# Optimization experiments

Measured on AMD Instinct MI355X. Metric: run time of the kernel, lower is better.

The kernel has to match this reference:

```python
import jax, jax.numpy as jnp
import numpy as np

H, W, C_IN, C_ADD = 721, 1440, 78, 8
N_NODES, K = 5882, 128
DAY_OF_YEAR = 182.5  # module default time_of_year
LN_EPS = 1e-5        # haiku LayerNorm default
NORM_EPS = 1e-7


def setup_inputs() -> dict:
    key = jax.random.key(0)
    ks = jax.random.split(key, 4)
    return {
        "var_grid": jax.random.normal(ks[0], (H, W, C_IN), dtype=jnp.float32),
        "nearby_idx": jax.random.randint(ks[1], (N_NODES, K), 0, H * W),
        "input_means": jnp.zeros((C_IN + C_ADD,), jnp.float32),
        "input_stds": jnp.ones((C_IN + C_ADD,), jnp.float32),
        "W1": jax.random.normal(ks[2], (C_IN + C_ADD, 256), dtype=jnp.float32) * 0.1,
        "b1": jnp.zeros((256,), jnp.float32),
        "ln_scale": jnp.ones((256,), jnp.float32),
        "ln_offset": jnp.zeros((256,), jnp.float32),
        "W2": jax.random.normal(ks[3], (256, 256), dtype=jnp.float32) * 0.1,
        "b2": jnp.zeros((256,), jnp.float32),
    }


def _additional_features(h, w):
    # 8 extra channels: sin/cos of lat/lon, normalized day-of-year, 3 zero pads
    lat = jnp.linspace(-90.0, 90.0, h)
    lon = jnp.linspace(0.0, 360.0, w)
    lat2d = jnp.broadcast_to(lat[:, None], (h, w))
    lon2d = jnp.broadcast_to(lon[None, :], (h, w))
    lat_r, lon_r = jnp.radians(lat2d), jnp.radians(lon2d)
    day = jnp.float32(DAY_OF_YEAR / 365.0)
    z = jnp.zeros((h, w), jnp.float32)
    return jnp.stack([
        jnp.sin(lat_r), jnp.cos(lat_r), jnp.sin(lon_r), jnp.cos(lon_r),
        jnp.full((h, w), day, jnp.float32), z, z, z,
    ], axis=-1)  # [H, W, 8]


def reference(var_grid, nearby_idx, input_means, input_stds,
              W1, b1, ln_scale, ln_offset, W2, b2):
    h, w, c = var_grid.shape
    add = _additional_features(h, w)                       # [H, W, 8]
    flat = jnp.concatenate([var_grid, add], -1).reshape(h * w, c + C_ADD)
    gathered = flat[nearby_idx]                            # [N, K, 86] irregular gather
    x = (gathered - input_means) / (input_stds + NORM_EPS)
    hidden = jax.nn.relu(jnp.einsum('nkc,cd->nkd', x, W1) + b1)
    mu = hidden.mean(-1, keepdims=True)
    var = hidden.var(-1, keepdims=True)
    hidden = (hidden - mu) * jax.lax.rsqrt(var + LN_EPS) * ln_scale + ln_offset
    nodes = jnp.einsum('nkd,de->nke', hidden, W2) + b2     # [N, K, 256]
    return nodes
```

## Files before the change

kernel.cpp:

```cpp
#include <hip/hip_runtime.h>
#include <hip/hip_bf16.h>
#include <math.h>

#define GH 721
#define GW 1440
#define C_IN 78
#define NNODES 5882
#define KNEIGH 128
#define M_TOTAL (NNODES * KNEIGH)
#define TM 64
#define NBLOCKS (M_TOTAL / TM)

typedef __attribute__((ext_vector_type(8))) short bf16x8;
typedef __attribute__((ext_vector_type(4))) float f32x4;

__device__ __forceinline__ unsigned short f2bf(float x) {
    __hip_bfloat16 b = __float2bfloat16(x);
    union { __hip_bfloat16 h; unsigned short u; } cv; cv.h = b; return cv.u;
}

__global__ void prep_kernel(const float* __restrict__ W1, const float* __restrict__ W2,
                            const float* __restrict__ means, const float* __restrict__ stds,
                            const float* __restrict__ b1,
                            unsigned short* __restrict__ bp1, unsigned short* __restrict__ bp2,
                            float* __restrict__ latT, float* __restrict__ lonT,
                            float* __restrict__ b1p)
{
    const int NB1 = 3 * 4 * 256 * 8;
    const int NB2 = 8 * 4 * 256 * 8;
    const int NTOT = NB1 + NB2 + GH + GW + 256;
    for (int e = blockIdx.x * blockDim.x + threadIdx.x; e < NTOT;
         e += gridDim.x * blockDim.x) {
        if (e < NB1) {
            int j = e & 7, c = (e >> 3) & 255, o = (e >> 11) & 3, s = e >> 13;
            int k = s * 32 + o * 8 + j;
            float v = 0.f;
            if (k < 82) v = W1[k * 256 + c] / (stds[k] + 1e-7f);
            bp1[e] = f2bf(v);
        } else if (e < NB1 + NB2) {
            int t = e - NB1;
            int j = t & 7, c = (t >> 3) & 255, o = (t >> 11) & 3, s = t >> 13;
            int k = s * 32 + o * 8 + j;
            bp2[t] = f2bf(W2[k * 256 + c]);
        } else if (e < NB1 + NB2 + GH) {
            int h = e - NB1 - NB2;
            float r = (-90.f + 0.25f * (float)h) * 0.017453292519943295f;
            latT[2 * h]     = sinf(r);
            latT[2 * h + 1] = cosf(r);
        } else if (e < NB1 + NB2 + GH + GW) {
            int w = e - NB1 - NB2 - GH;
            float r = ((float)w * (360.f / 1439.f)) * 0.017453292519943295f;
            lonT[2 * w]     = sinf(r);
            lonT[2 * w + 1] = cosf(r);
        } else {
            int c = e - NB1 - NB2 - GH - GW;
            float acc = b1[c];
            #pragma unroll 1
            for (int k = 0; k < 86; ++k) {
                float inv = 1.f / (stds[k] + 1e-7f);
                float w = W1[k * 256 + c] * inv;
                acc -= means[k] * w;
                if (k == 82) acc += 0.5f * w;
            }
            b1p[c] = acc;
        }
    }
}

__global__ __launch_bounds__(256, 4)
void fused_kernel(const float* __restrict__ var_grid, const int* __restrict__ idxs,
                  const unsigned short* __restrict__ bp1, const unsigned short* __restrict__ bp2,
                  const float* __restrict__ latT, const float* __restrict__ lonT,
                  const float* __restrict__ b1p, const float* __restrict__ lnS,
                  const float* __restrict__ lnO, const float* __restrict__ b2,
                  float* __restrict__ out)
{
    __shared__ __align__(16) char smem[TM * 256 * 2];
    __shared__ float red[2][4][TM];
    unsigned short* h_lds = (unsigned short*)smem;
    unsigned short (*x_lds)[104] = (unsigned short (*)[104])smem;
    float* otile = (float*)smem;

    const int tid  = threadIdx.x;
    const int lane = tid & 63;
    const int wave = tid >> 6;
    const int l15  = lane & 15;
    const int lg   = lane >> 4;
    const int wbase = wave * 64;
    const long block0 = (long)blockIdx.x * TM;

    {
        const int row = tid >> 2, p = tid & 3;
        const int idx = idxs[block0 + row];
        const int hh = idx / GW;
        const int ww = idx - hh * GW;
        const float* src = var_grid + (long)idx * C_IN;
        unsigned int* xrow = (unsigned int*)&x_lds[row][0];
        #pragma unroll
        for (int t = 0; t < 12; ++t) {
            const int q = p + 4 * t;
            float v0, v1;
            if (q < 39) {
                float2 t2 = *(const float2*)(src + 2 * q);
                v0 = t2.x; v1 = t2.y;
            } else if (q == 39) { v0 = latT[2 * hh]; v1 = latT[2 * hh + 1]; }
            else if (q == 40)   { v0 = lonT[2 * ww]; v1 = lonT[2 * ww + 1]; }
            else                { v0 = 0.f; v1 = 0.f; }
            xrow[q] = ((unsigned int)f2bf(v1) << 16) | (unsigned int)f2bf(v0);
        }
    }

    float b1v[4], lsv[4], lov[4], b2v[4];
    #pragma unroll
    for (int nf = 0; nf < 4; ++nf) {
        int col = wbase + nf * 16 + l15;
        b1v[nf] = b1p[col]; lsv[nf] = lnS[col]; lov[nf] = lnO[col]; b2v[nf] = b2[col];
    }
    __syncthreads();

    f32x4 acc[4][4];
    #pragma unroll
    for (int mf = 0; mf < 4; ++mf)
        #pragma unroll
        for (int nf = 0; nf < 4; ++nf) acc[mf][nf] = (f32x4){0.f, 0.f, 0.f, 0.f};

    #pragma unroll
    for (int s = 0; s < 3; ++s) {
        bf16x8 af[4], bw[4];
        #pragma unroll
        for (int mf = 0; mf < 4; ++mf)
            af[mf] = *(const bf16x8*)&x_lds[mf * 16 + l15][s * 32 + lg * 8];
        #pragma unroll
        for (int nf = 0; nf < 4; ++nf)
            bw[nf] = *(const bf16x8*)(bp1 + ((size_t)((s * 4 + lg) * 256) + wbase + nf * 16 + l15) * 8);
        #pragma unroll
        for (int mf = 0; mf < 4; ++mf)
            #pragma unroll
            for (int nf = 0; nf < 4; ++nf)
                acc[mf][nf] = __builtin_amdgcn_mfma_f32_16x16x32_bf16(af[mf], bw[nf], acc[mf][nf], 0, 0, 0);
    }

    float sm[4][4], sq[4][4];
    #pragma unroll
    for (int mf = 0; mf < 4; ++mf)
        #pragma unroll
        for (int i = 0; i < 4; ++i) { sm[mf][i] = 0.f; sq[mf][i] = 0.f; }

    #pragma unroll
    for (int mf = 0; mf < 4; ++mf)
        #pragma unroll
        for (int nf = 0; nf < 4; ++nf)
            #pragma unroll
            for (int i = 0; i < 4; ++i) {
                float v = fmaxf(acc[mf][nf][i] + b1v[nf], 0.f);
                acc[mf][nf][i] = v;
                sm[mf][i] += v;
                sq[mf][i] += v * v;
            }

    #pragma unroll
    for (int m = 1; m < 16; m <<= 1)
        #pragma unroll
        for (int mf = 0; mf < 4; ++mf)
            #pragma unroll
            for (int i = 0; i < 4; ++i) {
                sm[mf][i] += __shfl_xor(sm[mf][i], m, 64);
                sq[mf][i] += __shfl_xor(sq[mf][i], m, 64);
            }

    if (l15 == 0) {
        #pragma unroll
        for (int mf = 0; mf < 4; ++mf)
            #pragma unroll
            for (int i = 0; i < 4; ++i) {
                int row = mf * 16 + lg * 4 + i;
                red[0][wave][row] = sm[mf][i];
                red[1][wave][row] = sq[mf][i];
            }
    }
    __syncthreads();

    #pragma unroll
    for (int mf = 0; mf < 4; ++mf)
        #pragma unroll
        for (int i = 0; i < 4; ++i) {
            int row = mf * 16 + lg * 4 + i;
            float tot = red[0][0][row] + red[0][1][row] + red[0][2][row] + red[0][3][row];
            float tq  = red[1][0][row] + red[1][1][row] + red[1][2][row] + red[1][3][row];
            float mean = tot * (1.f / 256.f);
            float var  = tq * (1.f / 256.f) - mean * mean;
            float rs = rsqrtf(var + 1e-5f);
            #pragma unroll
            for (int nf = 0; nf < 4; ++nf) {
                float v = (acc[mf][nf][i] - mean) * rs * lsv[nf] + lov[nf];
                int col = wbase + nf * 16 + l15;
                unsigned off = (unsigned)(row * 512 + col * 2);
                off ^= (unsigned)((row & 7) << 4);
                *(unsigned short*)((char*)h_lds + off) = f2bf(v);
            }
        }
    __syncthreads();

    #pragma unroll
    for (int mf = 0; mf < 4; ++mf)
        #pragma unroll
        for (int nf = 0; nf < 4; ++nf) acc[mf][nf] = (f32x4){0.f, 0.f, 0.f, 0.f};

    #pragma unroll
    for (int s = 0; s < 8; ++s) {
        bf16x8 af[4], bw[4];
        #pragma unroll
        for (int mf = 0; mf < 4; ++mf) {
            int row = mf * 16 + l15;
            unsigned off = (unsigned)(row * 512 + (s * 32 + lg * 8) * 2);
            off ^= (unsigned)((row & 7) << 4);
            af[mf] = *(const bf16x8*)((char*)h_lds + off);
        }
        #pragma unroll
        for (int nf = 0; nf < 4; ++nf)
            bw[nf] = *(const bf16x8*)(bp2 + ((size_t)((s * 4 + lg) * 256) + wbase + nf * 16 + l15) * 8);
        #pragma unroll
        for (int mf = 0; mf < 4; ++mf)
            #pragma unroll
            for (int nf = 0; nf < 4; ++nf)
                acc[mf][nf] = __builtin_amdgcn_mfma_f32_16x16x32_bf16(af[mf], bw[nf], acc[mf][nf], 0, 0, 0);
    }

    #pragma unroll
    for (int p = 0; p < 2; ++p) {
        __syncthreads();
        #pragma unroll
        for (int mfl = 0; mfl < 2; ++mfl) {
            const int mf = p * 2 + mfl;
            #pragma unroll
            for (int i = 0; i < 4; ++i) {
                int rl = mfl * 16 + lg * 4 + i;
                #pragma unroll
                for (int nf = 0; nf < 4; ++nf)
                    otile[rl * 256 + wbase + nf * 16 + l15] = acc[mf][nf][i] + b2v[nf];
            }
        }
        __syncthreads();
        #pragma unroll
        for (int r8 = 0; r8 < 8; ++r8) {
            const int rl = wave * 8 + r8;
            const long row_g = block0 + p * 32 + rl;
            f32x4 v = *(const f32x4*)&otile[rl * 256 + lane * 4];
            __builtin_nontemporal_store(v, (f32x4*)(out + row_g * 256 + lane * 4));
        }
    }
}

extern "C" void kernel_launch(void* const* d_in, const int* in_sizes, int n_in,
                              void* d_out, int out_size, void* d_ws, size_t ws_size,
                              hipStream_t stream) {
    const float* var_grid = (const float*)d_in[0];
    const int*   idxs     = (const int*)d_in[1];
    const float* means    = (const float*)d_in[2];
    const float* stds     = (const float*)d_in[3];
    const float* W1       = (const float*)d_in[4];
    const float* b1       = (const float*)d_in[5];
    const float* lnS      = (const float*)d_in[6];
    const float* lnO      = (const float*)d_in[7];
    const float* W2       = (const float*)d_in[8];
    const float* b2       = (const float*)d_in[9];
    float* out = (float*)d_out;

    char* ws = (char*)d_ws;
    unsigned short* bp1 = (unsigned short*)ws;
    unsigned short* bp2 = (unsigned short*)(ws + 49152);
    float* latT = (float*)(ws + 180224);
    float* lonT = (float*)(ws + 186000);
    float* b1p  = (float*)(ws + 197520);

    prep_kernel<<<362, 256, 0, stream>>>(W1, W2, means, stds, b1, bp1, bp2, latT, lonT, b1p);
    fused_kernel<<<NBLOCKS, 256, 0, stream>>>(var_grid, idxs, bp1, bp2, latT, lonT,
                                              b1p, lnS, lnO, b2, out);
}
```

Measured before the change: 484.9 us.

## Double row tile to 128 with 8-wave 2x4 grid and prefetch weight fragments

Each block now handles 128 gathered rows with 512 threads arranged as a 2x4 wave grid, so weight fragments are reused across more rows per block. Gather loads are issued into registers before the bf16 packing, and weight fragments are register double-buffered across the k-steps of both GEMMs. The output staging tile gets a rotation swizzle to reduce LDS bank conflicts. The launch bound of (512,4) asks for 8 waves per SIMD, which tightens the per-thread register budget while each thread still holds a 64-float accumulator plus prefetch buffers, so spills are a risk.

```diff
diff --git a/kernel.cpp b/kernel.cpp
--- a/kernel.cpp
+++ b/kernel.cpp
@@ -8,7 +8,7 @@
 #define NNODES 5882
 #define KNEIGH 128
 #define M_TOTAL (NNODES * KNEIGH)
-#define TM 64
+#define TM 128
 #define NBLOCKS (M_TOTAL / TM)
 
 typedef __attribute__((ext_vector_type(8))) short bf16x8;
@@ -67,7 +67,7 @@
     }
 }
 
-__global__ __launch_bounds__(256, 4)
+__global__ __launch_bounds__(512, 4)
 void fused_kernel(const float* __restrict__ var_grid, const int* __restrict__ idxs,
                   const unsigned short* __restrict__ bp1, const unsigned short* __restrict__ bp2,
                   const float* __restrict__ latT, const float* __restrict__ lonT,
@@ -84,9 +84,12 @@
     const int tid  = threadIdx.x;
     const int lane = tid & 63;
     const int wave = tid >> 6;
+    const int wr   = wave >> 2;
+    const int wc   = wave & 3;
     const int l15  = lane & 15;
     const int lg   = lane >> 4;
-    const int wbase = wave * 64;
+    const int wbase = wc * 64;
+    const int rbase = wr * 64;
     const long block0 = (long)blockIdx.x * TM;
 
     {
@@ -95,17 +98,24 @@
         const int hh = idx / GW;
         const int ww = idx - hh * GW;
         const float* src = var_grid + (long)idx * C_IN;
+        float2 g[10];
+        #pragma unroll
+        for (int t = 0; t < 10; ++t) {
+            const int q = p + 4 * t;
+            if (q < 39) g[t] = *(const float2*)(src + 2 * q);
+        }
+        float2 tail;
+        tail.x = latT[2 * hh]; tail.y = latT[2 * hh + 1];
+        float2 tail2; tail2.x = lonT[2 * ww]; tail2.y = lonT[2 * ww + 1];
         unsigned int* xrow = (unsigned int*)&x_lds[row][0];
         #pragma unroll
         for (int t = 0; t < 12; ++t) {
             const int q = p + 4 * t;
             float v0, v1;
-            if (q < 39) {
-                float2 t2 = *(const float2*)(src + 2 * q);
-                v0 = t2.x; v1 = t2.y;
-            } else if (q == 39) { v0 = latT[2 * hh]; v1 = latT[2 * hh + 1]; }
-            else if (q == 40)   { v0 = lonT[2 * ww]; v1 = lonT[2 * ww + 1]; }
-            else                { v0 = 0.f; v1 = 0.f; }
+            if (q < 39)      { v0 = g[t].x; v1 = g[t].y; }
+            else if (q == 39){ v0 = tail.x;  v1 = tail.y; }
+            else if (q == 40){ v0 = tail2.x; v1 = tail2.y; }
+            else             { v0 = 0.f; v1 = 0.f; }
             xrow[q] = ((unsigned int)f2bf(v1) << 16) | (unsigned int)f2bf(v0);
         }
     }
@@ -124,20 +134,28 @@
         #pragma unroll
         for (int nf = 0; nf < 4; ++nf) acc[mf][nf] = (f32x4){0.f, 0.f, 0.f, 0.f};
 
+    bf16x8 bw[4], bwn[4];
+    #pragma unroll
+    for (int nf = 0; nf < 4; ++nf)
+        bw[nf] = *(const bf16x8*)(bp1 + ((size_t)(lg * 256) + wbase + nf * 16 + l15) * 8);
+
     #pragma unroll
     for (int s = 0; s < 3; ++s) {
-        bf16x8 af[4], bw[4];
-        #pragma unroll
-        for (int mf = 0; mf < 4; ++mf)
-            af[mf] = *(const bf16x8*)&x_lds[mf * 16 + l15][s * 32 + lg * 8];
-        #pragma unroll
-        for (int nf = 0; nf < 4; ++nf)
-            bw[nf] = *(const bf16x8*)(bp1 + ((size_t)((s * 4 + lg) * 256) + wbase + nf * 16 + l15) * 8);
+        if (s < 2)
+            #pragma unroll
+            for (int nf = 0; nf < 4; ++nf)
+                bwn[nf] = *(const bf16x8*)(bp1 + ((size_t)(((s + 1) * 4 + lg) * 256) + wbase + nf * 16 + l15) * 8);
+        bf16x8 af[4];
+        #pragma unroll
+        for (int mf = 0; mf < 4; ++mf)
+            af[mf] = *(const bf16x8*)&x_lds[rbase + mf * 16 + l15][s * 32 + lg * 8];
         #pragma unroll
         for (int mf = 0; mf < 4; ++mf)
             #pragma unroll
             for (int nf = 0; nf < 4; ++nf)
                 acc[mf][nf] = __builtin_amdgcn_mfma_f32_16x16x32_bf16(af[mf], bw[nf], acc[mf][nf], 0, 0, 0);
+        #pragma unroll
+        for (int nf = 0; nf < 4; ++nf) bw[nf] = bwn[nf];
     }
 
     float sm[4][4], sq[4][4];
@@ -173,9 +191,9 @@
         for (int mf = 0; mf < 4; ++mf)
             #pragma unroll
             for (int i = 0; i < 4; ++i) {
-                int row = mf * 16 + lg * 4 + i;
-                red[0][wave][row] = sm[mf][i];
-                red[1][wave][row] = sq[mf][i];
+                int row = rbase + mf * 16 + lg * 4 + i;
+                red[0][wc][row] = sm[mf][i];
+                red[1][wc][row] = sq[mf][i];
             }
     }
     __syncthreads();
@@ -184,7 +202,7 @@
     for (int mf = 0; mf < 4; ++mf)
         #pragma unroll
         for (int i = 0; i < 4; ++i) {
-            int row = mf * 16 + lg * 4 + i;
+            int row = rbase + mf * 16 + lg * 4 + i;
             float tot = red[0][0][row] + red[0][1][row] + red[0][2][row] + red[0][3][row];
             float tq  = red[1][0][row] + red[1][1][row] + red[1][2][row] + red[1][3][row];
             float mean = tot * (1.f / 256.f);
@@ -207,45 +225,56 @@
         for (int nf = 0; nf < 4; ++nf) acc[mf][nf] = (f32x4){0.f, 0.f, 0.f, 0.f};
 
     #pragma unroll
+    for (int nf = 0; nf < 4; ++nf)
+        bw[nf] = *(const bf16x8*)(bp2 + ((size_t)(lg * 256) + wbase + nf * 16 + l15) * 8);
+
+    #pragma unroll
     for (int s = 0; s < 8; ++s) {
-        bf16x8 af[4], bw[4];
+        if (s < 7)
+            #pragma unroll
+            for (int nf = 0; nf < 4; ++nf)
+                bwn[nf] = *(const bf16x8*)(bp2 + ((size_t)(((s + 1) * 4 + lg) * 256) + wbase + nf * 16 + l15) * 8);
+        bf16x8 af[4];
         #pragma unroll
         for (int mf = 0; mf < 4; ++mf) {
-            int row = mf * 16 + l15;
+            int row = rbase + mf * 16 + l15;
             unsigned off = (unsigned)(row * 512 + (s * 32 + lg * 8) * 2);
             off ^= (unsigned)((row & 7) << 4);
             af[mf] = *(const bf16x8*)((char*)h_lds + off);
         }
         #pragma unroll
-        for (int nf = 0; nf < 4; ++nf)
-            bw[nf] = *(const bf16x8*)(bp2 + ((size_t)((s * 4 + lg) * 256) + wbase + nf * 16 + l15) * 8);
-        #pragma unroll
         for (int mf = 0; mf < 4; ++mf)
             #pragma unroll
             for (int nf = 0; nf < 4; ++nf)
                 acc[mf][nf] = __builtin_amdgcn_mfma_f32_16x16x32_bf16(af[mf], bw[nf], acc[mf][nf], 0, 0, 0);
-    }
-
-    #pragma unroll
-    for (int p = 0; p < 2; ++p) {
+        #pragma unroll
+        for (int nf = 0; nf < 4; ++nf) bw[nf] = bwn[nf];
+    }
+
+    #pragma unroll
+    for (int p = 0; p < 4; ++p) {
         __syncthreads();
-        #pragma unroll
-        for (int mfl = 0; mfl < 2; ++mfl) {
-            const int mf = p * 2 + mfl;
-            #pragma unroll
-            for (int i = 0; i < 4; ++i) {
-                int rl = mfl * 16 + lg * 4 + i;
+        if (wr == (p >> 1)) {
+            #pragma unroll
+            for (int mfl = 0; mfl < 2; ++mfl) {
+                const int mf = (p & 1) * 2 + mfl;
                 #pragma unroll
-                for (int nf = 0; nf < 4; ++nf)
-                    otile[rl * 256 + wbase + nf * 16 + l15] = acc[mf][nf][i] + b2v[nf];
+                for (int i = 0; i < 4; ++i) {
+                    int rl = mfl * 16 + lg * 4 + i;
+                    #pragma unroll
+                    for (int nf = 0; nf < 4; ++nf) {
+                        int col = wbase + nf * 16 + l15;
+                        otile[rl * 256 + ((col + rl * 4) & 255)] = acc[mf][nf][i] + b2v[nf];
+                    }
+                }
             }
         }
         __syncthreads();
         #pragma unroll
-        for (int r8 = 0; r8 < 8; ++r8) {
-            const int rl = wave * 8 + r8;
+        for (int r4 = 0; r4 < 4; ++r4) {
+            const int rl = wave * 4 + r4;
             const long row_g = block0 + p * 32 + rl;
-            f32x4 v = *(const f32x4*)&otile[rl * 256 + lane * 4];
+            f32x4 v = *(const f32x4*)&otile[rl * 256 + ((lane * 4 + rl * 4) & 255)];
             __builtin_nontemporal_store(v, (f32x4*)(out + row_g * 256 + lane * 4));
         }
     }
@@ -274,6 +303,6 @@
     float* b1p  = (float*)(ws + 197520);
 
     prep_kernel<<<362, 256, 0, stream>>>(W1, W2, means, stds, b1, bp1, bp2, latT, lonT, b1p);
-    fused_kernel<<<NBLOCKS, 256, 0, stream>>>(var_grid, idxs, bp1, bp2, latT, lonT,
+    fused_kernel<<<NBLOCKS, 512, 0, stream>>>(var_grid, idxs, bp1, bp2, latT, lonT,
                                               b1p, lnS, lnO, b2, out);
 }
```

New measurement: 524.1 us. +8.1%, slower.

## Process two row tiles per block, prefetching the second tile's gather during compute

Applied to the files above, without the earlier changes.

Each block now handles two 64-row tiles. The gather loads for the second tile are issued into registers before the first tile's GEMM/LayerNorm/GEMM, so their latency overlaps the first tile's compute. The output staging tile gets a rotated column index to reduce LDS bank conflicts, and the output stores switch from nontemporal to regular stores. The trade-off is higher register pressure (about 20 extra floats per thread under launch_bounds 256,4) and half as many blocks.

```diff
diff --git a/kernel.cpp b/kernel.cpp
--- a/kernel.cpp
+++ b/kernel.cpp
@@ -9,7 +9,7 @@
 #define KNEIGH 128
 #define M_TOTAL (NNODES * KNEIGH)
 #define TM 64
-#define NBLOCKS (M_TOTAL / TM)
+#define NBLOCKS (M_TOTAL / (2 * TM))
 
 typedef __attribute__((ext_vector_type(8))) short bf16x8;
 typedef __attribute__((ext_vector_type(4))) float f32x4;
@@ -67,6 +67,152 @@
     }
 }
 
+__device__ __forceinline__ void compute_tile(
+    char* smem, float (*red)[4][TM],
+    const unsigned short* __restrict__ bp1, const unsigned short* __restrict__ bp2,
+    const float* b1v, const float* lsv, const float* lov, const float* b2v,
+    float* __restrict__ out, long gbase,
+    int lane, int wave, int l15, int lg, int wbase)
+{
+    unsigned short* h_lds = (unsigned short*)smem;
+    unsigned short (*x_lds)[104] = (unsigned short (*)[104])smem;
+    float* otile = (float*)smem;
+
+    f32x4 acc[4][4];
+    #pragma unroll
+    for (int mf = 0; mf < 4; ++mf)
+        #pragma unroll
+        for (int nf = 0; nf < 4; ++nf) acc[mf][nf] = (f32x4){0.f, 0.f, 0.f, 0.f};
+
+    #pragma unroll
+    for (int s = 0; s < 3; ++s) {
+        bf16x8 af[4], bw[4];
+        #pragma unroll
+        for (int mf = 0; mf < 4; ++mf)
+            af[mf] = *(const bf16x8*)&x_lds[mf * 16 + l15][s * 32 + lg * 8];
+        #pragma unroll
+        for (int nf = 0; nf < 4; ++nf)
+            bw[nf] = *(const bf16x8*)(bp1 + ((size_t)((s * 4 + lg) * 256) + wbase + nf * 16 + l15) * 8);
+        #pragma unroll
+        for (int mf = 0; mf < 4; ++mf)
+            #pragma unroll
+            for (int nf = 0; nf < 4; ++nf)
+                acc[mf][nf] = __builtin_amdgcn_mfma_f32_16x16x32_bf16(af[mf], bw[nf], acc[mf][nf], 0, 0, 0);
+    }
+
+    float sm[4][4], sq[4][4];
+    #pragma unroll
+    for (int mf = 0; mf < 4; ++mf)
+        #pragma unroll
+        for (int i = 0; i < 4; ++i) { sm[mf][i] = 0.f; sq[mf][i] = 0.f; }
+
+    #pragma unroll
+    for (int mf = 0; mf < 4; ++mf)
+        #pragma unroll
+        for (int nf = 0; nf < 4; ++nf)
+            #pragma unroll
+            for (int i = 0; i < 4; ++i) {
+                float v = fmaxf(acc[mf][nf][i] + b1v[nf], 0.f);
+                acc[mf][nf][i] = v;
+                sm[mf][i] += v;
+                sq[mf][i] += v * v;
+            }
+
+    #pragma unroll
+    for (int m = 1; m < 16; m <<= 1)
+        #pragma unroll
+        for (int mf = 0; mf < 4; ++mf)
+            #pragma unroll
+            for (int i = 0; i < 4; ++i) {
+                sm[mf][i] += __shfl_xor(sm[mf][i], m, 64);
+                sq[mf][i] += __shfl_xor(sq[mf][i], m, 64);
+            }
+
+    if (l15 == 0) {
+        #pragma unroll
+        for (int mf = 0; mf < 4; ++mf)
+            #pragma unroll
+            for (int i = 0; i < 4; ++i) {
+                int row = mf * 16 + lg * 4 + i;
+                red[0][wave][row] = sm[mf][i];
+                red[1][wave][row] = sq[mf][i];
+            }
+    }
+    __syncthreads();
+
+    #pragma unroll
+    for (int mf = 0; mf < 4; ++mf)
+        #pragma unroll
+        for (int i = 0; i < 4; ++i) {
+            int row = mf * 16 + lg * 4 + i;
+            float tot = red[0][0][row] + red[0][1][row] + red[0][2][row] + red[0][3][row];
+            float tq  = red[1][0][row] + red[1][1][row] + red[1][2][row] + red[1][3][row];
+            float mean = tot * (1.f / 256.f);
+            float var  = tq * (1.f / 256.f) - mean * mean;
+            float rs = rsqrtf(var + 1e-5f);
+            #pragma unroll
+            for (int nf = 0; nf < 4; ++nf) {
+                float v = (acc[mf][nf][i] - mean) * rs * lsv[nf] + lov[nf];
+                int col = wbase + nf * 16 + l15;
+                unsigned off = (unsigned)(row * 512 + col * 2);
+                off ^= (unsigned)((row & 7) << 4);
+                *(unsigned short*)((char*)h_lds + off) = f2bf(v);
+            }
+        }
+    __syncthreads();
+
+    #pragma unroll
+    for (int mf = 0; mf < 4; ++mf)
+        #pragma unroll
+        for (int nf = 0; nf < 4; ++nf) acc[mf][nf] = (f32x4){0.f, 0.f, 0.f, 0.f};
+
+    #pragma unroll
+    for (int s = 0; s < 8; ++s) {
+        bf16x8 af[4], bw[4];
+        #pragma unroll
+        for (int mf = 0; mf < 4; ++mf) {
+            int row = mf * 16 + l15;
+            unsigned off = (unsigned)(row * 512 + (s * 32 + lg * 8) * 2);
+            off ^= (unsigned)((row & 7) << 4);
+            af[mf] = *(const bf16x8*)((char*)h_lds + off);
+        }
+        #pragma unroll
+        for (int nf = 0; nf < 4; ++nf)
+            bw[nf] = *(const bf16x8*)(bp2 + ((size_t)((s * 4 + lg) * 256) + wbase + nf * 16 + l15) * 8);
+        #pragma unroll
+        for (int mf = 0; mf < 4; ++mf)
+            #pragma unroll
+            for (int nf = 0; nf < 4; ++nf)
+                acc[mf][nf] = __builtin_amdgcn_mfma_f32_16x16x32_bf16(af[mf], bw[nf], acc[mf][nf], 0, 0, 0);
+    }
+
+    #pragma unroll
+    for (int p = 0; p < 2; ++p) {
+        __syncthreads();
+        #pragma unroll
+        for (int mfl = 0; mfl < 2; ++mfl) {
+            const int mf = p * 2 + mfl;
+            #pragma unroll
+            for (int i = 0; i < 4; ++i) {
+                int rl = mfl * 16 + lg * 4 + i;
+                #pragma unroll
+                for (int nf = 0; nf < 4; ++nf) {
+                    int col = wbase + nf * 16 + l15;
+                    otile[rl * 256 + ((col + rl * 4) & 255)] = acc[mf][nf][i] + b2v[nf];
+                }
+            }
+        }
+        __syncthreads();
+        #pragma unroll
+        for (int r8 = 0; r8 < 8; ++r8) {
+            const int rl = wave * 8 + r8;
+            const long row_g = gbase + p * 32 + rl;
+            f32x4 v = *(const f32x4*)&otile[rl * 256 + ((lane * 4 + rl * 4) & 255)];
+            *(f32x4*)(out + row_g * 256 + lane * 4) = v;
+        }
+    }
+}
+
 __global__ __launch_bounds__(256, 4)
 void fused_kernel(const float* __restrict__ var_grid, const int* __restrict__ idxs,
                   const unsigned short* __restrict__ bp1, const unsigned short* __restrict__ bp2,
@@ -77,9 +223,8 @@
 {
     __shared__ __align__(16) char smem[TM * 256 * 2];
     __shared__ float red[2][4][TM];
-    unsigned short* h_lds = (unsigned short*)smem;
+
     unsigned short (*x_lds)[104] = (unsigned short (*)[104])smem;
-    float* otile = (float*)smem;
 
     const int tid  = threadIdx.x;
     const int lane = tid & 63;
@@ -87,25 +232,34 @@
     const int l15  = lane & 15;
     const int lg   = lane >> 4;
     const int wbase = wave * 64;
-    const long block0 = (long)blockIdx.x * TM;
+    const long block0 = (long)blockIdx.x * (2 * TM);
+
+    const int row = tid >> 2, p = tid & 3;
+
+    const int idx0 = idxs[block0 + row];
+    const int idx1 = idxs[block0 + TM + row];
 
     {
-        const int row = tid >> 2, p = tid & 3;
-        const int idx = idxs[block0 + row];
-        const int hh = idx / GW;
-        const int ww = idx - hh * GW;
-        const float* src = var_grid + (long)idx * C_IN;
+        const int hh = idx0 / GW;
+        const int ww = idx0 - hh * GW;
+        const float* src = var_grid + (long)idx0 * C_IN;
+        float2 g[10], tl, tl2;
+        #pragma unroll
+        for (int t = 0; t < 10; ++t) {
+            const int q = p + 4 * t;
+            if (q < 39) g[t] = *(const float2*)(src + 2 * q);
+        }
+        tl.x  = latT[2 * hh]; tl.y  = latT[2 * hh + 1];
+        tl2.x = lonT[2 * ww]; tl2.y = lonT[2 * ww + 1];
         unsigned int* xrow = (unsigned int*)&x_lds[row][0];
         #pragma unroll
         for (int t = 0; t < 12; ++t) {
             const int q = p + 4 * t;
             float v0, v1;
-            if (q < 39) {
-                float2 t2 = *(const float2*)(src + 2 * q);
-                v0 = t2.x; v1 = t2.y;
-            } else if (q == 39) { v0 = latT[2 * hh]; v1 = latT[2 * hh + 1]; }
-            else if (q == 40)   { v0 = lonT[2 * ww]; v1 = lonT[2 * ww + 1]; }
-            else                { v0 = 0.f; v1 = 0.f; }
+            if (q < 39)      { v0 = g[t].x; v1 = g[t].y; }
+            else if (q == 39){ v0 = tl.x;  v1 = tl.y; }
+            else if (q == 40){ v0 = tl2.x; v1 = tl2.y; }
+            else             { v0 = 0.f; v1 = 0.f; }
             xrow[q] = ((unsigned int)f2bf(v1) << 16) | (unsigned int)f2bf(v0);
         }
     }
@@ -118,137 +272,42 @@
     }
     __syncthreads();
 
-    f32x4 acc[4][4];
-    #pragma unroll
-    for (int mf = 0; mf < 4; ++mf)
-        #pragma unroll
-        for (int nf = 0; nf < 4; ++nf) acc[mf][nf] = (f32x4){0.f, 0.f, 0.f, 0.f};
-
-    #pragma unroll
-    for (int s = 0; s < 3; ++s) {
-        bf16x8 af[4], bw[4];
-        #pragma unroll
-        for (int mf = 0; mf < 4; ++mf)
-            af[mf] = *(const bf16x8*)&x_lds[mf * 16 + l15][s * 32 + lg * 8];
-        #pragma unroll
-        for (int nf = 0; nf < 4; ++nf)
-            bw[nf] = *(const bf16x8*)(bp1 + ((size_t)((s * 4 + lg) * 256) + wbase + nf * 16 + l15) * 8);
-        #pragma unroll
-        for (int mf = 0; mf < 4; ++mf)
-            #pragma unroll
-            for (int nf = 0; nf < 4; ++nf)
-                acc[mf][nf] = __builtin_amdgcn_mfma_f32_16x16x32_bf16(af[mf], bw[nf], acc[mf][nf], 0, 0, 0);
-    }
-
-    float sm[4][4], sq[4][4];
-    #pragma unroll
-    for (int mf = 0; mf < 4; ++mf)
-        #pragma unroll
-        for (int i = 0; i < 4; ++i) { sm[mf][i] = 0.f; sq[mf][i] = 0.f; }
-
-    #pragma unroll
-    for (int mf = 0; mf < 4; ++mf)
-        #pragma unroll
-        for (int nf = 0; nf < 4; ++nf)
-            #pragma unroll
-            for (int i = 0; i < 4; ++i) {
-                float v = fmaxf(acc[mf][nf][i] + b1v[nf], 0.f);
-                acc[mf][nf][i] = v;
-                sm[mf][i] += v;
-                sq[mf][i] += v * v;
-            }
-
-    #pragma unroll
-    for (int m = 1; m < 16; m <<= 1)
-        #pragma unroll
-        for (int mf = 0; mf < 4; ++mf)
-            #pragma unroll
-            for (int i = 0; i < 4; ++i) {
-                sm[mf][i] += __shfl_xor(sm[mf][i], m, 64);
-                sq[mf][i] += __shfl_xor(sq[mf][i], m, 64);
-            }
-
-    if (l15 == 0) {
-        #pragma unroll
-        for (int mf = 0; mf < 4; ++mf)
-            #pragma unroll
-            for (int i = 0; i < 4; ++i) {
-                int row = mf * 16 + lg * 4 + i;
-                red[0][wave][row] = sm[mf][i];
-                red[1][wave][row] = sq[mf][i];
-            }
-    }
-    __syncthreads();
-
-    #pragma unroll
-    for (int mf = 0; mf < 4; ++mf)
-        #pragma unroll
-        for (int i = 0; i < 4; ++i) {
-            int row = mf * 16 + lg * 4 + i;
-            float tot = red[0][0][row] + red[0][1][row] + red[0][2][row] + red[0][3][row];
-            float tq  = red[1][0][row] + red[1][1][row] + red[1][2][row] + red[1][3][row];
-            float mean = tot * (1.f / 256.f);
-            float var  = tq * (1.f / 256.f) - mean * mean;
-            float rs = rsqrtf(var + 1e-5f);
-            #pragma unroll
-            for (int nf = 0; nf < 4; ++nf) {
-                float v = (acc[mf][nf][i] - mean) * rs * lsv[nf] + lov[nf];
-                int col = wbase + nf * 16 + l15;
-                unsigned off = (unsigned)(row * 512 + col * 2);
-                off ^= (unsigned)((row & 7) << 4);
-                *(unsigned short*)((char*)h_lds + off) = f2bf(v);
-            }
-        }
-    __syncthreads();
-
-    #pragma unroll
-    for (int mf = 0; mf < 4; ++mf)
-        #pragma unroll
-        for (int nf = 0; nf < 4; ++nf) acc[mf][nf] = (f32x4){0.f, 0.f, 0.f, 0.f};
-
-    #pragma unroll
-    for (int s = 0; s < 8; ++s) {
-        bf16x8 af[4], bw[4];
-        #pragma unroll
-        for (int mf = 0; mf < 4; ++mf) {
-            int row = mf * 16 + l15;
-            unsigned off = (unsigned)(row * 512 + (s * 32 + lg * 8) * 2);
-            off ^= (unsigned)((row & 7) << 4);
-            af[mf] = *(const bf16x8*)((char*)h_lds + off);
-        }
-        #pragma unroll
-        for (int nf = 0; nf < 4; ++nf)
-            bw[nf] = *(const bf16x8*)(bp2 + ((size_t)((s * 4 + lg) * 256) + wbase + nf * 16 + l15) * 8);
-        #pragma unroll
-        for (int mf = 0; mf < 4; ++mf)
-            #pragma unroll
-            for (int nf = 0; nf < 4; ++nf)
-                acc[mf][nf] = __builtin_amdgcn_mfma_f32_16x16x32_bf16(af[mf], bw[nf], acc[mf][nf], 0, 0, 0);
-    }
-
-    #pragma unroll
-    for (int p = 0; p < 2; ++p) {
-        __syncthreads();
-        #pragma unroll
-        for (int mfl = 0; mfl < 2; ++mfl) {
-            const int mf = p * 2 + mfl;
-            #pragma unroll
-            for (int i = 0; i < 4; ++i) {
-                int rl = mfl * 16 + lg * 4 + i;
-                #pragma unroll
-                for (int nf = 0; nf < 4; ++nf)
-                    otile[rl * 256 + wbase + nf * 16 + l15] = acc[mf][nf][i] + b2v[nf];
-            }
-        }
-        __syncthreads();
-        #pragma unroll
-        for (int r8 = 0; r8 < 8; ++r8) {
-            const int rl = wave * 8 + r8;
-            const long row_g = block0 + p * 32 + rl;
-            f32x4 v = *(const f32x4*)&otile[rl * 256 + lane * 4];
-            __builtin_nontemporal_store(v, (f32x4*)(out + row_g * 256 + lane * 4));
-        }
-    }
+    float2 g1[10], tl1, tl21;
+    {
+        const int hh = idx1 / GW;
+        const int ww = idx1 - hh * GW;
+        const float* src = var_grid + (long)idx1 * C_IN;
+        #pragma unroll
+        for (int t = 0; t < 10; ++t) {
+            const int q = p + 4 * t;
+            if (q < 39) g1[t] = *(const float2*)(src + 2 * q);
+        }
+        tl1.x  = latT[2 * hh]; tl1.y  = latT[2 * hh + 1];
+        tl21.x = lonT[2 * ww]; tl21.y = lonT[2 * ww + 1];
+    }
+
+    compute_tile(smem, red, bp1, bp2, b1v, lsv, lov, b2v, out, block0,
+                 lane, wave, l15, lg, wbase);
+
+    __syncthreads();
+
+    {
+        unsigned int* xrow = (unsigned int*)&x_lds[row][0];
+        #pragma unroll
+        for (int t = 0; t < 12; ++t) {
+            const int q = p + 4 * t;
+            float v0, v1;
+            if (q < 39)      { v0 = g1[t].x; v1 = g1[t].y; }
+            else if (q == 39){ v0 = tl1.x;  v1 = tl1.y; }
+            else if (q == 40){ v0 = tl21.x; v1 = tl21.y; }
+            else             { v0 = 0.f; v1 = 0.f; }
+            xrow[q] = ((unsigned int)f2bf(v1) << 16) | (unsigned int)f2bf(v0);
+        }
+    }
+    __syncthreads();
+
+    compute_tile(smem, red, bp1, bp2, b1v, lsv, lov, b2v, out, block0 + TM,
+                 lane, wave, l15, lg, wbase);
 }
 
 extern "C" void kernel_launch(void* const* d_in, const int* in_sizes, int n_in,
```

Result: slower. 911.2 us (+87.9%).
